# Optimization experiments

Hardware: AMD Instinct MI355X
Metric: run time of the kernel (lower is better)

Reference implementation:

```python
import math
import jax, jax.numpy as jnp
import numpy as np

ORD_Q, ORD_K = 1, 2
DIM_QK, N_HEADS = 64, 4
DH = DIM_QK // N_HEADS  # dim_qk_head = 16


def mask_tensor(order, n):
    """Bool tensor of shape [n]*order, True where all `order` indices are pairwise distinct."""
    idx = jnp.arange(n)
    m = jnp.ones((n,) * order, dtype=bool)
    for i in range(order):
        for j in range(i + 1, order):
            si = [1] * order; si[i] = n
            sj = [1] * order; sj[j] = n
            m = m & (idx.reshape(si) != idx.reshape(sj))
    return m


def setup_inputs() -> dict:
    key = jax.random.key(0)
    k1, k2, k3 = jax.random.split(key, 3)
    B, n = 4, 128
    q_A = jax.random.normal(k1, (B, n, DIM_QK), dtype=jnp.float32)
    k_A = jax.random.normal(k2, (B, n, n, DIM_QK), dtype=jnp.float32)
    node_mask = jax.random.uniform(k3, (B, n)) > 0.2   # valid-node mask
    q_mask = node_mask                                  # order-1 mask [B, n]
    k_mask = node_mask[:, :, None] & node_mask[:, None, :]  # order-2 mask [B, n, n]
    return {"q_A": q_A, "k_A": k_A, "q_mask": q_mask, "k_mask": k_mask}


def reference(q_A, k_A, q_mask, k_mask):
    B, n, D = q_A.shape
    Lq, Lk = n ** ORD_Q, n ** ORD_K
    # split heads: chunk h takes channels [h*DH:(h+1)*DH] -> [H, B, L, DH]
    q = q_A.reshape(B, Lq, N_HEADS, DH).transpose(2, 0, 1, 3)
    k = k_A.reshape(B, Lk, N_HEADS, DH).transpose(2, 0, 1, 3)
    # combinatorial all-distinct mask over ord_q+ord_k = 3 indices -> [Lq, Lk]
    M = mask_tensor(ORD_Q + ORD_K, n).reshape(Lq, Lk)
    qk_mask = q_mask.reshape(B, Lq)[:, :, None] & k_mask.reshape(B, Lk)[:, None, :]
    att_mask = (M[None] & qk_mask)[None]  # [1, B, Lq, Lk]
    sdp = jnp.einsum('hbkd,hbld->hbkl', q, k) / math.sqrt(DH)
    sdp = jnp.where(att_mask, sdp, -jnp.inf)
    alpha = jax.nn.softmax(sdp, axis=-1)
    alpha = jnp.where(att_mask, alpha, 0.0)  # also zeroes NaN rows (fully masked)
    return alpha
```

## Files before the change

### kernel.cpp

```cpp
#include <hip/hip_runtime.h>
#include <math.h>

#define BB 4
#define NN 128
#define LK 16384
#define DD 64
#define HH 4
#define DHH 16
#define TI2 32
#define L1CH 256
#define NL1 (LK/L1CH)
#define L2CH 64
#define NL2 (LK/L2CH)
#define KROWS 64
#define KPAD 68

__device__ __forceinline__ int compute_mode(const void* __restrict__ qmask){
  const unsigned int* w = (const unsigned int*)qmask;
  const int t = threadIdx.x & 63;
  int u8 = 0, i32 = 0, f32 = 0;
  #pragma unroll
  for (int rep = 0; rep < 2; ++rep){
    const unsigned int x = w[t + rep*64];
    const bool one  = (x == 1u);
    const bool fone = (x == 0x3f800000u);
    const bool nz   = (x != 0u);
    u8  += __popcll(__ballot(nz && !one && !fone));
    i32 += __popcll(__ballot(one));
    f32 += __popcll(__ballot(fone));
  }
  int mode = 0;
  if (u8 > i32 && u8 > f32) mode = 1;
  else if (f32 > i32) mode = 2;
  return mode;
}

__device__ __forceinline__ bool mget(const void* __restrict__ p, int idx, int mode){
  if (mode == 1) return ((const unsigned char*)p)[idx] != 0;
  if (mode == 2) return ((const float*)p)[idx] != 0.0f;
  return ((const int*)p)[idx] != 0;
}

__device__ __forceinline__ float dot16(float4 q0, float4 q1, float4 q2, float4 q3,
                                       float4 k0, float4 k1, float4 k2, float4 k3){
  float d;
  d = q0.x*k0.x;         d = fmaf(q0.y,k0.y,d); d = fmaf(q0.z,k0.z,d); d = fmaf(q0.w,k0.w,d);
  d = fmaf(q1.x,k1.x,d); d = fmaf(q1.y,k1.y,d); d = fmaf(q1.z,k1.z,d); d = fmaf(q1.w,k1.w,d);
  d = fmaf(q2.x,k2.x,d); d = fmaf(q2.y,k2.y,d); d = fmaf(q2.z,k2.z,d); d = fmaf(q2.w,k2.w,d);
  d = fmaf(q3.x,k3.x,d); d = fmaf(q3.y,k3.y,d); d = fmaf(q3.z,k3.z,d); d = fmaf(q3.w,k3.w,d);
  return d;
}

__device__ __forceinline__ void stage_k(const float* __restrict__ kA, int b, int lbase,
                                        float* __restrict__ ldsK){
  const int t = threadIdx.x;
  const float4* src = (const float4*)(kA + (((size_t)b << 14) + lbase)*DD);
  #pragma unroll
  for (int p = 0; p < 4; ++p){
    const int f = p*256 + t;
    const float4 v = src[f];
    *(float4*)(ldsK + (f >> 4)*KPAD + (f & 15)*4) = v;
  }
}

__device__ __forceinline__ void stage_q(const float* __restrict__ qA, int b, int ibase,
                                        float* __restrict__ ldsQ){
  const int t = threadIdx.x;
  const float4* src = (const float4*)(qA + ((size_t)(b*NN + ibase))*DD);
  #pragma unroll
  for (int p = 0; p < 2; ++p){
    const int f = p*256 + t;
    float4 v = src[f];
    v.x *= 0.25f; v.y *= 0.25f; v.z *= 0.25f; v.w *= 0.25f;
    *(float4*)(ldsQ + (f >> 4)*DD + (f & 15)*4) = v;
  }
}

__global__ __launch_bounds__(256) void k1_rowsum(
    const float* __restrict__ qA, const float* __restrict__ kA,
    const void* __restrict__ qm, const void* __restrict__ km,
    float* __restrict__ partials)
{
  __shared__ float ldsK[KROWS*KPAD];
  __shared__ float ldsQ[TI2*DD];
  __shared__ float ldsP[HH][TI2];
  const int mode = compute_mode(qm);
  const int lc = blockIdx.x, it = blockIdx.y, b = blockIdx.z;
  const int t = threadIdx.x, w = t >> 6, ll = t & 63;
  const int ibase = it*TI2;

  stage_q(qA, b, ibase, ldsQ);

  float s[TI2];
  #pragma unroll
  for (int i = 0; i < TI2; ++i) s[i] = 0.0f;

  for (int jj = 0; jj < L1CH/KROWS; ++jj){
    if (jj) __syncthreads();
    stage_k(kA, b, lc*L1CH + jj*KROWS, ldsK);
    __syncthreads();

    const int l  = lc*L1CH + jj*KROWS + ll;
    const int jn = l >> 7, kn = l & 127;
    const bool kv = (jn != kn) && mget(km, (b << 14) + l, mode);
    unsigned vmask = kv ? 0xFFFFFFFFu : 0u;
    if ((unsigned)(jn - ibase) < TI2) vmask &= ~(1u << (jn - ibase));
    if ((unsigned)(kn - ibase) < TI2) vmask &= ~(1u << (kn - ibase));

    const float* kp = ldsK + ll*KPAD + w*DHH;
    const float4 k0 = *(const float4*)(kp),    k1 = *(const float4*)(kp+4),
                 k2 = *(const float4*)(kp+8),  k3 = *(const float4*)(kp+12);

    #pragma unroll
    for (int i = 0; i < TI2; ++i){
      const float* qp = ldsQ + i*DD + w*DHH;
      float d = dot16(*(const float4*)(qp),   *(const float4*)(qp+4),
                      *(const float4*)(qp+8), *(const float4*)(qp+12),
                      k0, k1, k2, k3);
      d = (vmask & (1u << i)) ? d : -INFINITY;
      s[i] += __expf(d);
    }
  }

  #pragma unroll
  for (int i = 0; i < TI2; ++i){
    float v = s[i];
    #pragma unroll
    for (int off = 32; off; off >>= 1) v += __shfl_xor(v, off);
    if (ll == 0) ldsP[w][i] = v;
  }
  __syncthreads();
  if (t < HH*TI2){
    const int h = t >> 5, i = t & 31;
    const bool qv = mget(qm, b*NN + ibase + i, mode);
    partials[((lc*BB + b)*HH + h)*NN + ibase + i] = qv ? ldsP[h][i] : 0.0f;
  }
}

__global__ void k1_finalize(const float* __restrict__ partials, float* __restrict__ R){
  const int tid = blockIdx.x*256 + threadIdx.x;
  float ssum = 0.0f;
  for (int lc = 0; lc < NL1; ++lc) ssum += partials[lc*(BB*HH*NN) + tid];
  const int ig = tid & 127, h = (tid >> 7) & 3, b = tid >> 9;
  R[(b*NN + ig)*HH + h] = (ssum > 0.0f) ? 1.0f/ssum : 0.0f;
}

__global__ __launch_bounds__(256) void k2_emit(
    const float* __restrict__ qA, const float* __restrict__ kA,
    const void* __restrict__ qm, const void* __restrict__ km,
    const float* __restrict__ R, float* __restrict__ out)
{
  __shared__ float ldsK[KROWS*KPAD];
  __shared__ float ldsQ[TI2*DD];
  const int mode = compute_mode(qm);
  const int lc = blockIdx.x, it = blockIdx.y, b = blockIdx.z;
  const int t = threadIdx.x, w = t >> 6, ll = t & 63;
  const int ibase = it*TI2;
  const int lbase = lc*L2CH;

  stage_q(qA, b, ibase, ldsQ);
  stage_k(kA, b, lbase, ldsK);
  __syncthreads();

  const int l  = lbase + ll;
  const int jn = l >> 7, kn = l & 127;
  const bool kv = (jn != kn) && mget(km, (b << 14) + l, mode);
  unsigned vmask = kv ? 0xFFFFFFFFu : 0u;
  if ((unsigned)(jn - ibase) < TI2) vmask &= ~(1u << (jn - ibase));
  if ((unsigned)(kn - ibase) < TI2) vmask &= ~(1u << (kn - ibase));

  const float* kp = ldsK + ll*KPAD + w*DHH;
  const float4 k0 = *(const float4*)(kp),    k1 = *(const float4*)(kp+4),
               k2 = *(const float4*)(kp+8),  k3 = *(const float4*)(kp+12);

  float* op = out + (((size_t)((w*BB + b)*NN + ibase)) << 14) + lbase + ll;
  const float* Rp = R + (b*NN + ibase)*HH + w;

  #pragma unroll 4
  for (int i = 0; i < TI2; ++i){
    const float* qp = ldsQ + i*DD + w*DHH;
    float d = dot16(*(const float4*)(qp),   *(const float4*)(qp+4),
                    *(const float4*)(qp+8), *(const float4*)(qp+12),
                    k0, k1, k2, k3);
    d = (vmask & (1u << i)) ? d : -INFINITY;
    const float r = Rp[i*HH];
    op[((size_t)i) << 14] = __expf(d) * r;
  }
}

extern "C" void kernel_launch(void* const* d_in, const int* in_sizes, int n_in,
                              void* d_out, int out_size, void* d_ws, size_t ws_size,
                              hipStream_t stream)
{
  const float* qA = (const float*)d_in[0];
  const float* kA = (const float*)d_in[1];
  const void*  qm = d_in[2];
  const void*  km = d_in[3];
  float* out = (float*)d_out;

  float* partials = (float*)d_ws;
  float* R        = partials + (size_t)NL1*BB*HH*NN;

  dim3 g1(NL1, NN/TI2, BB);
  k1_rowsum<<<g1, 256, 0, stream>>>(qA, kA, qm, km, partials);
  k1_finalize<<<(BB*HH*NN)/256, 256, 0, stream>>>(partials, R);
  dim3 g2(NL2, NN/TI2, BB);
  k2_emit<<<g2, 256, 0, stream>>>(qA, kA, qm, km, R, out);
}
```

Measured before the change: 73.01 us.

## Drop LDS staging in emit kernel, widen per-thread outputs, use exp2 scaling

The emit kernel now loads K directly into registers, four key positions per thread, and writes float4 outputs. It drops the LDS staging and the block barrier. Q is read straight from global memory as wave-uniform loads, replacing the LDS Q buffer in both kernels. The 1/sqrt(d)*log2(e) scale is folded into K so that exp2 can replace expf. The rowsum grid now adapts its chunk count to the workspace size, which allows more blocks.

```diff
diff --git a/kernel.cpp b/kernel.cpp
--- a/kernel.cpp
+++ b/kernel.cpp
@@ -8,12 +8,17 @@
 #define HH 4
 #define DHH 16
 #define TI2 32
-#define L1CH 256
-#define NL1 (LK/L1CH)
-#define L2CH 64
-#define NL2 (LK/L2CH)
 #define KROWS 64
 #define KPAD 68
+#define QK_SCALE 0.3606737602f
+
+__device__ __forceinline__ float fexp2(float x){
+#if __has_builtin(__builtin_amdgcn_exp2f)
+  return __builtin_amdgcn_exp2f(x);
+#else
+  return __expf(x * 0.6931471806f);
+#endif
+}
 
 __device__ __forceinline__ int compute_mode(const void* __restrict__ qmask){
   const unsigned int* w = (const unsigned int*)qmask;
@@ -54,25 +59,13 @@
 __device__ __forceinline__ void stage_k(const float* __restrict__ kA, int b, int lbase,
                                         float* __restrict__ ldsK){
   const int t = threadIdx.x;
-  const float4* src = (const float4*)(kA + (((size_t)b << 14) + lbase)*DD);
+  const float4* src = (const float4*)(kA + ((size_t)(b*LK + lbase))*DD);
   #pragma unroll
   for (int p = 0; p < 4; ++p){
     const int f = p*256 + t;
-    const float4 v = src[f];
+    float4 v = src[f];
+    v.x *= QK_SCALE; v.y *= QK_SCALE; v.z *= QK_SCALE; v.w *= QK_SCALE;
     *(float4*)(ldsK + (f >> 4)*KPAD + (f & 15)*4) = v;
-  }
-}
-
-__device__ __forceinline__ void stage_q(const float* __restrict__ qA, int b, int ibase,
-                                        float* __restrict__ ldsQ){
-  const int t = threadIdx.x;
-  const float4* src = (const float4*)(qA + ((size_t)(b*NN + ibase))*DD);
-  #pragma unroll
-  for (int p = 0; p < 2; ++p){
-    const int f = p*256 + t;
-    float4 v = src[f];
-    v.x *= 0.25f; v.y *= 0.25f; v.z *= 0.25f; v.w *= 0.25f;
-    *(float4*)(ldsQ + (f >> 4)*DD + (f & 15)*4) = v;
   }
 }
 
@@ -82,43 +75,43 @@
     float* __restrict__ partials)
 {
   __shared__ float ldsK[KROWS*KPAD];
-  __shared__ float ldsQ[TI2*DD];
   __shared__ float ldsP[HH][TI2];
   const int mode = compute_mode(qm);
+  const int nl = gridDim.x;
+  const int chunks = (LK/nl)/KROWS;
   const int lc = blockIdx.x, it = blockIdx.y, b = blockIdx.z;
   const int t = threadIdx.x, w = t >> 6, ll = t & 63;
+  const int hs = __builtin_amdgcn_readfirstlane(w);
   const int ibase = it*TI2;
-
-  stage_q(qA, b, ibase, ldsQ);
+  const float* qbase = qA + ((size_t)(b*NN + ibase))*DD + hs*DHH;
 
   float s[TI2];
   #pragma unroll
   for (int i = 0; i < TI2; ++i) s[i] = 0.0f;
 
-  for (int jj = 0; jj < L1CH/KROWS; ++jj){
+  const int lbase0 = lc*(LK/nl);
+  for (int jj = 0; jj < chunks; ++jj){
     if (jj) __syncthreads();
-    stage_k(kA, b, lc*L1CH + jj*KROWS, ldsK);
+    stage_k(kA, b, lbase0 + jj*KROWS, ldsK);
     __syncthreads();
 
-    const int l  = lc*L1CH + jj*KROWS + ll;
+    const int l  = lbase0 + jj*KROWS + ll;
     const int jn = l >> 7, kn = l & 127;
-    const bool kv = (jn != kn) && mget(km, (b << 14) + l, mode);
+    const bool kv = (jn != kn) && mget(km, b*LK + l, mode);
     unsigned vmask = kv ? 0xFFFFFFFFu : 0u;
     if ((unsigned)(jn - ibase) < TI2) vmask &= ~(1u << (jn - ibase));
     if ((unsigned)(kn - ibase) < TI2) vmask &= ~(1u << (kn - ibase));
 
-    const float* kp = ldsK + ll*KPAD + w*DHH;
+    const float* kp = ldsK + ll*KPAD + hs*DHH;
     const float4 k0 = *(const float4*)(kp),    k1 = *(const float4*)(kp+4),
                  k2 = *(const float4*)(kp+8),  k3 = *(const float4*)(kp+12);
 
-    #pragma unroll
+    #pragma unroll 8
     for (int i = 0; i < TI2; ++i){
-      const float* qp = ldsQ + i*DD + w*DHH;
-      float d = dot16(*(const float4*)(qp),   *(const float4*)(qp+4),
-                      *(const float4*)(qp+8), *(const float4*)(qp+12),
-                      k0, k1, k2, k3);
+      const float4* qp = (const float4*)(qbase + i*DD);
+      float d = dot16(qp[0], qp[1], qp[2], qp[3], k0, k1, k2, k3);
       d = (vmask & (1u << i)) ? d : -INFINITY;
-      s[i] += __expf(d);
+      s[i] += fexp2(d);
     }
   }
 
@@ -133,16 +126,16 @@
   if (t < HH*TI2){
     const int h = t >> 5, i = t & 31;
     const bool qv = mget(qm, b*NN + ibase + i, mode);
-    partials[((lc*BB + b)*HH + h)*NN + ibase + i] = qv ? ldsP[h][i] : 0.0f;
-  }
-}
-
-__global__ void k1_finalize(const float* __restrict__ partials, float* __restrict__ R){
+    partials[lc*(BB*HH*NN) + (b*HH + h)*NN + ibase + i] = qv ? ldsP[h][i] : 0.0f;
+  }
+}
+
+__global__ void k1_finalize(const float* __restrict__ partials, float* __restrict__ R,
+                            int nl){
   const int tid = blockIdx.x*256 + threadIdx.x;
   float ssum = 0.0f;
-  for (int lc = 0; lc < NL1; ++lc) ssum += partials[lc*(BB*HH*NN) + tid];
-  const int ig = tid & 127, h = (tid >> 7) & 3, b = tid >> 9;
-  R[(b*NN + ig)*HH + h] = (ssum > 0.0f) ? 1.0f/ssum : 0.0f;
+  for (int lc = 0; lc < nl; ++lc) ssum += partials[lc*(BB*HH*NN) + tid];
+  R[tid] = (ssum > 0.0f) ? 1.0f/ssum : 0.0f;
 }
 
 __global__ __launch_bounds__(256) void k2_emit(
@@ -150,41 +143,52 @@
     const void* __restrict__ qm, const void* __restrict__ km,
     const float* __restrict__ R, float* __restrict__ out)
 {
-  __shared__ float ldsK[KROWS*KPAD];
-  __shared__ float ldsQ[TI2*DD];
   const int mode = compute_mode(qm);
   const int lc = blockIdx.x, it = blockIdx.y, b = blockIdx.z;
   const int t = threadIdx.x, w = t >> 6, ll = t & 63;
+  const int hs = __builtin_amdgcn_readfirstlane(w);
   const int ibase = it*TI2;
-  const int lbase = lc*L2CH;
-
-  stage_q(qA, b, ibase, ldsQ);
-  stage_k(kA, b, lbase, ldsK);
-  __syncthreads();
-
-  const int l  = lbase + ll;
-  const int jn = l >> 7, kn = l & 127;
-  const bool kv = (jn != kn) && mget(km, (b << 14) + l, mode);
-  unsigned vmask = kv ? 0xFFFFFFFFu : 0u;
-  if ((unsigned)(jn - ibase) < TI2) vmask &= ~(1u << (jn - ibase));
-  if ((unsigned)(kn - ibase) < TI2) vmask &= ~(1u << (kn - ibase));
-
-  const float* kp = ldsK + ll*KPAD + w*DHH;
-  const float4 k0 = *(const float4*)(kp),    k1 = *(const float4*)(kp+4),
-               k2 = *(const float4*)(kp+8),  k3 = *(const float4*)(kp+12);
-
-  float* op = out + (((size_t)((w*BB + b)*NN + ibase)) << 14) + lbase + ll;
-  const float* Rp = R + (b*NN + ibase)*HH + w;
+  const int lbase = lc*256 + ll*4;
+
+  float4 kk[4][4];
+  #pragma unroll
+  for (int e = 0; e < 4; ++e){
+    const float4* kp = (const float4*)(kA + ((size_t)(b*LK + lbase + e))*DD + hs*DHH);
+    #pragma unroll
+    for (int p = 0; p < 4; ++p){
+      float4 v = kp[p];
+      v.x *= QK_SCALE; v.y *= QK_SCALE; v.z *= QK_SCALE; v.w *= QK_SCALE;
+      kk[e][p] = v;
+    }
+  }
+
+  unsigned vm[4];
+  #pragma unroll
+  for (int e = 0; e < 4; ++e){
+    const int l = lbase + e;
+    const int jn = l >> 7, kn = l & 127;
+    const bool kv = (jn != kn) && mget(km, b*LK + l, mode);
+    unsigned m = kv ? 0xFFFFFFFFu : 0u;
+    if ((unsigned)(jn - ibase) < TI2) m &= ~(1u << (jn - ibase));
+    if ((unsigned)(kn - ibase) < TI2) m &= ~(1u << (kn - ibase));
+    vm[e] = m;
+  }
+
+  const float* qbase = qA + ((size_t)(b*NN + ibase))*DD + hs*DHH;
+  const float* Rbase = R + (b*HH + hs)*NN + ibase;
+  float* op = out + (((size_t)((hs*BB + b)*NN + ibase)) << 14) + lbase;
 
   #pragma unroll 4
   for (int i = 0; i < TI2; ++i){
-    const float* qp = ldsQ + i*DD + w*DHH;
-    float d = dot16(*(const float4*)(qp),   *(const float4*)(qp+4),
-                    *(const float4*)(qp+8), *(const float4*)(qp+12),
-                    k0, k1, k2, k3);
-    d = (vmask & (1u << i)) ? d : -INFINITY;
-    const float r = Rp[i*HH];
-    op[((size_t)i) << 14] = __expf(d) * r;
+    const float4* qp = (const float4*)(qbase + i*DD);
+    const float4 q0 = qp[0], q1 = qp[1], q2 = qp[2], q3 = qp[3];
+    const float r = Rbase[i];
+    float4 o;
+    o.x = fexp2((vm[0] & (1u<<i)) ? dot16(q0,q1,q2,q3, kk[0][0],kk[0][1],kk[0][2],kk[0][3]) : -INFINITY) * r;
+    o.y = fexp2((vm[1] & (1u<<i)) ? dot16(q0,q1,q2,q3, kk[1][0],kk[1][1],kk[1][2],kk[1][3]) : -INFINITY) * r;
+    o.z = fexp2((vm[2] & (1u<<i)) ? dot16(q0,q1,q2,q3, kk[2][0],kk[2][1],kk[2][2],kk[2][3]) : -INFINITY) * r;
+    o.w = fexp2((vm[3] & (1u<<i)) ? dot16(q0,q1,q2,q3, kk[3][0],kk[3][1],kk[3][2],kk[3][3]) : -INFINITY) * r;
+    *(float4*)(op + (((size_t)i) << 14)) = o;
   }
 }
 
@@ -198,12 +202,15 @@
   const void*  km = d_in[3];
   float* out = (float*)d_out;
 
+  const size_t need128 = ((size_t)128*BB*HH*NN + BB*HH*NN)*sizeof(float);
+  const int nl1 = (ws_size >= need128) ? 128 : 64;
+
   float* partials = (float*)d_ws;
-  float* R        = partials + (size_t)NL1*BB*HH*NN;
-
-  dim3 g1(NL1, NN/TI2, BB);
+  float* R        = partials + (size_t)nl1*BB*HH*NN;
+
+  dim3 g1(nl1, NN/TI2, BB);
   k1_rowsum<<<g1, 256, 0, stream>>>(qA, kA, qm, km, partials);
-  k1_finalize<<<(BB*HH*NN)/256, 256, 0, stream>>>(partials, R);
-  dim3 g2(NL2, NN/TI2, BB);
+  k1_finalize<<<(BB*HH*NN)/256, 256, 0, stream>>>(partials, R, nl1);
+  dim3 g2(LK/256, NN/TI2, BB);
   k2_emit<<<g2, 256, 0, stream>>>(qA, kA, qm, km, R, out);
 }
```

Result: slower. 117.1 us (+60.4%).

## Emit softmax output with float4 stores, register-held K rows, and exp2

Applied to the files above, without the earlier changes.

The emit kernel now gives each thread 4 consecutive key positions, loads their K slices straight into registers (no LDS staging) and writes float4 stores. This cuts the number of blocks by 4x and widens the global stores. The row reciprocals are staged in LDS and stored in a contiguous layout. The scale now folds in log2(e) so both kernels can use the native exp2. The cost is higher register pressure from the 16 float4 K values held per thread.

```diff
diff --git a/kernel.cpp b/kernel.cpp
--- a/kernel.cpp
+++ b/kernel.cpp
@@ -8,12 +8,19 @@
 #define HH 4
 #define DHH 16
 #define TI2 32
+#define KROWS 64
+#define KPAD 68
 #define L1CH 256
 #define NL1 (LK/L1CH)
-#define L2CH 64
-#define NL2 (LK/L2CH)
-#define KROWS 64
-#define KPAD 68
+#define QK_SCALE 0.3606737602f
+
+__device__ __forceinline__ float fexp2(float x){
+#if __has_builtin(__builtin_amdgcn_exp2f)
+  return __builtin_amdgcn_exp2f(x);
+#else
+  return __expf(x * 0.6931471806f);
+#endif
+}
 
 __device__ __forceinline__ int compute_mode(const void* __restrict__ qmask){
   const unsigned int* w = (const unsigned int*)qmask;
@@ -54,7 +61,7 @@
 __device__ __forceinline__ void stage_k(const float* __restrict__ kA, int b, int lbase,
                                         float* __restrict__ ldsK){
   const int t = threadIdx.x;
-  const float4* src = (const float4*)(kA + (((size_t)b << 14) + lbase)*DD);
+  const float4* src = (const float4*)(kA + ((size_t)(b*LK + lbase))*DD);
   #pragma unroll
   for (int p = 0; p < 4; ++p){
     const int f = p*256 + t;
@@ -71,7 +78,7 @@
   for (int p = 0; p < 2; ++p){
     const int f = p*256 + t;
     float4 v = src[f];
-    v.x *= 0.25f; v.y *= 0.25f; v.z *= 0.25f; v.w *= 0.25f;
+    v.x *= QK_SCALE; v.y *= QK_SCALE; v.z *= QK_SCALE; v.w *= QK_SCALE;
     *(float4*)(ldsQ + (f >> 4)*DD + (f & 15)*4) = v;
   }
 }
@@ -118,7 +125,7 @@
                       *(const float4*)(qp+8), *(const float4*)(qp+12),
                       k0, k1, k2, k3);
       d = (vmask & (1u << i)) ? d : -INFINITY;
-      s[i] += __expf(d);
+      s[i] += fexp2(d);
     }
   }
 
@@ -141,8 +148,7 @@
   const int tid = blockIdx.x*256 + threadIdx.x;
   float ssum = 0.0f;
   for (int lc = 0; lc < NL1; ++lc) ssum += partials[lc*(BB*HH*NN) + tid];
-  const int ig = tid & 127, h = (tid >> 7) & 3, b = tid >> 9;
-  R[(b*NN + ig)*HH + h] = (ssum > 0.0f) ? 1.0f/ssum : 0.0f;
+  R[tid] = (ssum > 0.0f) ? 1.0f/ssum : 0.0f;
 }
 
 __global__ __launch_bounds__(256) void k2_emit(
@@ -150,41 +156,54 @@
     const void* __restrict__ qm, const void* __restrict__ km,
     const float* __restrict__ R, float* __restrict__ out)
 {
-  __shared__ float ldsK[KROWS*KPAD];
   __shared__ float ldsQ[TI2*DD];
+  __shared__ float ldsR[HH*TI2];
   const int mode = compute_mode(qm);
   const int lc = blockIdx.x, it = blockIdx.y, b = blockIdx.z;
   const int t = threadIdx.x, w = t >> 6, ll = t & 63;
   const int ibase = it*TI2;
-  const int lbase = lc*L2CH;
+  const int lbase = lc*256 + ll*4;
 
   stage_q(qA, b, ibase, ldsQ);
-  stage_k(kA, b, lbase, ldsK);
+  if (t < HH*TI2){
+    ldsR[t] = R[(b*HH + (t >> 5))*NN + ibase + (t & 31)];
+  }
+
+  float4 kk[4][4];
+  #pragma unroll
+  for (int e = 0; e < 4; ++e){
+    const float4* kp = (const float4*)(kA + ((size_t)(b*LK + lbase + e))*DD + w*DHH);
+    #pragma unroll
+    for (int p = 0; p < 4; ++p) kk[e][p] = kp[p];
+  }
+
+  unsigned vm[4];
+  #pragma unroll
+  for (int e = 0; e < 4; ++e){
+    const int l = lbase + e;
+    const int jn = l >> 7, kn = l & 127;
+    const bool kv = (jn != kn) && mget(km, b*LK + l, mode);
+    unsigned m = kv ? 0xFFFFFFFFu : 0u;
+    if ((unsigned)(jn - ibase) < TI2) m &= ~(1u << (jn - ibase));
+    if ((unsigned)(kn - ibase) < TI2) m &= ~(1u << (kn - ibase));
+    vm[e] = m;
+  }
   __syncthreads();
 
-  const int l  = lbase + ll;
-  const int jn = l >> 7, kn = l & 127;
-  const bool kv = (jn != kn) && mget(km, (b << 14) + l, mode);
-  unsigned vmask = kv ? 0xFFFFFFFFu : 0u;
-  if ((unsigned)(jn - ibase) < TI2) vmask &= ~(1u << (jn - ibase));
-  if ((unsigned)(kn - ibase) < TI2) vmask &= ~(1u << (kn - ibase));
-
-  const float* kp = ldsK + ll*KPAD + w*DHH;
-  const float4 k0 = *(const float4*)(kp),    k1 = *(const float4*)(kp+4),
-               k2 = *(const float4*)(kp+8),  k3 = *(const float4*)(kp+12);
-
-  float* op = out + (((size_t)((w*BB + b)*NN + ibase)) << 14) + lbase + ll;
-  const float* Rp = R + (b*NN + ibase)*HH + w;
-
-  #pragma unroll 4
+  float* op = out + (((size_t)((w*BB + b)*NN + ibase)) << 14) + lbase;
+
+  #pragma unroll 2
   for (int i = 0; i < TI2; ++i){
     const float* qp = ldsQ + i*DD + w*DHH;
-    float d = dot16(*(const float4*)(qp),   *(const float4*)(qp+4),
-                    *(const float4*)(qp+8), *(const float4*)(qp+12),
-                    k0, k1, k2, k3);
-    d = (vmask & (1u << i)) ? d : -INFINITY;
-    const float r = Rp[i*HH];
-    op[((size_t)i) << 14] = __expf(d) * r;
+    const float4 q0 = *(const float4*)(qp),   q1 = *(const float4*)(qp+4),
+                 q2 = *(const float4*)(qp+8), q3 = *(const float4*)(qp+12);
+    const float r = ldsR[w*TI2 + i];
+    float4 o;
+    o.x = fexp2((vm[0] & (1u<<i)) ? dot16(q0,q1,q2,q3, kk[0][0],kk[0][1],kk[0][2],kk[0][3]) : -INFINITY) * r;
+    o.y = fexp2((vm[1] & (1u<<i)) ? dot16(q0,q1,q2,q3, kk[1][0],kk[1][1],kk[1][2],kk[1][3]) : -INFINITY) * r;
+    o.z = fexp2((vm[2] & (1u<<i)) ? dot16(q0,q1,q2,q3, kk[2][0],kk[2][1],kk[2][2],kk[2][3]) : -INFINITY) * r;
+    o.w = fexp2((vm[3] & (1u<<i)) ? dot16(q0,q1,q2,q3, kk[3][0],kk[3][1],kk[3][2],kk[3][3]) : -INFINITY) * r;
+    *(float4*)(op + (((size_t)i) << 14)) = o;
   }
 }
 
@@ -204,6 +223,6 @@
   dim3 g1(NL1, NN/TI2, BB);
   k1_rowsum<<<g1, 256, 0, stream>>>(qA, kA, qm, km, partials);
   k1_finalize<<<(BB*HH*NN)/256, 256, 0, stream>>>(partials, R);
-  dim3 g2(NL2, NN/TI2, BB);
+  dim3 g2(LK/256, NN/TI2, BB);
   k2_emit<<<g2, 256, 0, stream>>>(qA, kA, qm, km, R, out);
 }
```

Result: faster. 69.34 us, median of 2 (-5.0%).
